# Kernel optimization log

Hardware: AMD Instinct MI355X
Metric: run time of the kernel (lower is better)

Reference implementation:

```python
import jax, jax.numpy as jnp
import numpy as np

EPS = 1e-5
HEADS = 4
DQK = 128
DV = 128
SCALE = DQK ** -0.5


def _bn(x, g, b, m, v):
    # inference-mode BatchNorm over channel dim (axis=1)
    inv = g / jnp.sqrt(v + EPS)
    return x * inv[None, :, None, None] + (b - m * inv)[None, :, None, None]


def setup_inputs() -> dict:
    key = jax.random.key(0)
    ks = jax.random.split(key, 16)
    f = lambda i, shape, s=1.0: jax.random.normal(ks[i], shape, dtype=jnp.float32) * s
    N, Cin, H, W = 16, 2048, 32, 32
    mid = HEADS * DV  # 512
    return {
        "x": f(0, (N, Cin, H, W)),
        "conv1_w": f(1, (mid, Cin), 0.02),
        "gamma1": 1.0 + f(2, (mid,), 0.02),
        "beta1": f(3, (mid,), 0.02),
        "mean1": f(4, (mid,), 0.02),
        "var1": 1.0 + 0.1 * jax.random.uniform(ks[5], (mid,), dtype=jnp.float32),
        "qk_w": f(6, (2 * HEADS * DQK, mid), 0.02),
        "v_w": f(7, (HEADS * DV, mid), 0.02),
        "pos_h": f(8, (H, DQK), SCALE),
        "pos_w": f(9, (W, DQK), SCALE),
        "conv3_w": f(10, (Cin, mid), 0.02),
        "gamma3": 1.0 + f(11, (Cin,), 0.02),
        "beta3": f(12, (Cin,), 0.02),
        "mean3": f(13, (Cin,), 0.02),
        "var3": 1.0 + 0.1 * jax.random.uniform(ks[14], (Cin,), dtype=jnp.float32),
    }


def reference(x, conv1_w, gamma1, beta1, mean1, var1, qk_w, v_w, pos_h, pos_w,
              conv3_w, gamma3, beta3, mean3, var3):
    n, c, h, w = x.shape
    # conv1 (1x1) + BN + ReLU
    out = jnp.einsum('nchw,oc->nohw', x, conv1_w)
    out = jax.nn.relu(_bn(out, gamma1, beta1, mean1, var1))
    # MHSA
    qk = jnp.einsum('nchw,oc->nohw', out, qk_w)  # [n, 2*heads*dqk, h, w]
    vv = jnp.einsum('nchw,oc->nohw', out, v_w)   # [n, heads*dv, h, w]
    q, k = jnp.split(qk, 2, axis=1)

    def to_heads(t):
        d = t.shape[1] // HEADS
        return t.reshape(n, HEADS, d, h * w).transpose(0, 1, 3, 2)  # [n, H, hw, d]

    q, k, vv = to_heads(q), to_heads(k), to_heads(vv)
    q = q * SCALE
    # absolute positional embedding: emb[(h w), d]
    emb = (pos_h[:, None, :] + pos_w[None, :, :]).reshape(h * w, DQK)
    logits = jnp.einsum('nhxd,nhyd->nhxy', q, k) + jnp.einsum('nhxd,yd->nhxy', q, emb)
    weights = jax.nn.softmax(logits, axis=-1)
    attn = jnp.einsum('nhxy,nhyd->nhxd', weights, vv)  # [n, H, hw, dv]
    attn = attn.transpose(0, 1, 3, 2).reshape(n, HEADS * DV, h, w)
    # stride=1 -> avg_pool is identity
    attn = jax.nn.relu(attn)
    # conv3 (1x1) + BN
    out = jnp.einsum('nchw,oc->nohw', attn, conv3_w)
    out = _bn(out, gamma3, beta3, mean3, var3)
    # residual (downsample=None, in==out channels, stride=1) + ReLU
    return jax.nn.relu(out + x)
```

## Files before the change

kernel.cpp:

```cpp
#include <hip/hip_runtime.h>
#include <stdint.h>

typedef __bf16 bf16_t;
typedef __bf16 bf16x8 __attribute__((ext_vector_type(8)));
typedef float f32x4 __attribute__((ext_vector_type(4)));

#define EPSV 1e-5f
#define QSCALE 0.08838834764831845f
#define NB 16
#define HWD 1024
#define CIN 2048
#define MID 512
#define QKLD 1024

__device__ __forceinline__ void gl_lds16(const bf16_t* g, void* l) {
    __builtin_amdgcn_global_load_lds(
        (const __attribute__((address_space(1))) uint32_t*)g,
        (__attribute__((address_space(3))) uint32_t*)l, 16, 0, 0);
}

__device__ __forceinline__ f32x4 mfma16(bf16x8 a, bf16x8 b, f32x4 c) {
    return __builtin_amdgcn_mfma_f32_16x16x32_bf16(a, b, c, 0, 0, 0);
}

#define PW1 (512*2048)
#define PQK (PW1 + 1024*512)
#define PV  (PQK + 512*512)
#define PW3 (PV  + 2048*512)
#define PE  (PW3 + 1024*128)

__global__ void prep_kernel(const float* __restrict__ conv1_w,
                            const float* __restrict__ qk_w,
                            const float* __restrict__ v_w,
                            const float* __restrict__ pos_h,
                            const float* __restrict__ pos_w,
                            const float* __restrict__ conv3_w,
                            bf16_t* __restrict__ w1b, bf16_t* __restrict__ wqkb,
                            bf16_t* __restrict__ wvb, bf16_t* __restrict__ w3b,
                            float* __restrict__ emb) {
    int stride = gridDim.x * blockDim.x;
    for (int i = blockIdx.x * blockDim.x + threadIdx.x; i < PE; i += stride) {
        if (i < PW1) {
            w1b[i] = (bf16_t)conv1_w[i];
        } else if (i < PQK) {
            int j = i - PW1;
            int row = j >> 9;
            float v = (row < 512) ? qk_w[j] * QSCALE : qk_w[j];
            wqkb[j] = (bf16_t)v;
        } else if (i < PV) {
            int j = i - PQK;
            wvb[j] = (bf16_t)v_w[j];
        } else if (i < PW3) {
            int j = i - PV;
            w3b[j] = (bf16_t)conv3_w[j];
        } else {
            int j = i - PW3;
            int y = j >> 7, d = j & 127;
            emb[j] = pos_h[(y >> 5) * 128 + d] + pos_w[(y & 31) * 128 + d];
        }
    }
}

__global__ void transpose_x_kernel(const float* __restrict__ x, bf16_t* __restrict__ xt) {
    __shared__ uint32_t tileT[64][20];
    const int n = blockIdx.z;
    const int c0 = blockIdx.x * 32;
    const int hw0 = blockIdx.y * 64;
    const int t = threadIdx.x;

    const int cp = t >> 4;
    const int hw4 = (t & 15) * 4;
    const float* p0 = x + ((size_t)n * CIN + c0 + 2 * cp) * HWD + hw0 + hw4;
    const float4 a = *(const float4*)p0;
    const float4 b = *(const float4*)(p0 + HWD);
    float av[4] = {a.x, a.y, a.z, a.w};
    float bv[4] = {b.x, b.y, b.z, b.w};
#pragma unroll
    for (int i = 0; i < 4; ++i) {
        uint16_t lo = __builtin_bit_cast(uint16_t, (bf16_t)av[i]);
        uint16_t hi = __builtin_bit_cast(uint16_t, (bf16_t)bv[i]);
        tileT[hw4 + i][cp] = (uint32_t)lo | ((uint32_t)hi << 16);
    }
    __syncthreads();
    const int hw = t >> 2;
    const int seg = (t & 3) * 4;
    uint4 v = *(const uint4*)&tileT[hw][seg];
    *(uint4*)(xt + ((size_t)n * HWD + hw0 + hw) * CIN + c0 + 2 * seg) = v;
}

template <int EPI>
__global__ __launch_bounds__(256, 4)
void gemm_bt(const bf16_t* __restrict__ A, long long aStride,
             const bf16_t* __restrict__ B, long long bStride,
             int K, int ldc,
             const float* __restrict__ e0, const float* __restrict__ e1,
             const float* __restrict__ e2, const float* __restrict__ e3,
             const float* __restrict__ e4, long long e4Stride,
             void* __restrict__ C, long long cStride) {
    __shared__ f32x4 smemv[2048];
    char* smem = (char*)smemv;
    bf16_t* As = (bf16_t*)smem;
    bf16_t* Bs = (bf16_t*)(smem + 16384);
    const int lane = threadIdx.x & 63;
    const int wave = threadIdx.x >> 6;
    const int tN = blockIdx.x * 128, tM = blockIdx.y * 128;
    const int b = blockIdx.z;
    A += (size_t)b * aStride;
    B += (size_t)b * bStride;

    const int wm = (wave >> 1) * 64, wn = (wave & 1) * 64;
    const int lrow = lane & 15, quad = lane >> 4;
    const int srow = lane >> 3;
    const int sgr = lane & 7;
    const int lg = sgr ^ srow;

    f32x4 acc[4][4];
    const f32x4 z4 = {0.f, 0.f, 0.f, 0.f};
#pragma unroll
    for (int i = 0; i < 4; ++i)
#pragma unroll
        for (int j = 0; j < 4; ++j) acc[i][j] = z4;

    for (int k0 = 0; k0 < K; k0 += 64) {
        __syncthreads();
#pragma unroll
        for (int j = 0; j < 4; ++j) {
            const int blk = wave * 4 + j;
            const int row = blk * 8 + srow;
            gl_lds16(A + (size_t)(tM + row) * K + k0 + lg * 8,
                     (char*)As + blk * 1024 + lane * 16);
            gl_lds16(B + (size_t)(tN + row) * K + k0 + lg * 8,
                     (char*)Bs + blk * 1024 + lane * 16);
        }
        __syncthreads();
#pragma unroll
        for (int kh = 0; kh < 2; ++kh) {
            bf16x8 af[4], bfr[4];
#pragma unroll
            for (int t = 0; t < 4; ++t) {
                const int ar = wm + t * 16 + lrow;
                af[t] = *(const bf16x8*)(As + ar * 64 + (((kh * 4 + quad) ^ (ar & 7)) * 8));
                const int br = wn + t * 16 + lrow;
                bfr[t] = *(const bf16x8*)(Bs + br * 64 + (((kh * 4 + quad) ^ (br & 7)) * 8));
            }
#pragma unroll
            for (int i = 0; i < 4; ++i)
#pragma unroll
                for (int j = 0; j < 4; ++j)
                    acc[i][j] = mfma16(af[i], bfr[j], acc[i][j]);
        }
    }

    __syncthreads();
    float* Es = (float*)(smem + wave * 4352);
    const int pr = lane >> 3;
    const int pc = (lane & 7) * 8;
    const int gcol = tN + wn + pc;

#pragma unroll
    for (int i = 0; i < 4; ++i) {
#pragma unroll
        for (int j = 0; j < 4; ++j)
#pragma unroll
            for (int r = 0; r < 4; ++r)
                Es[(quad * 4 + r) * 68 + j * 16 + lrow] = acc[i][j][r];
#pragma unroll
        for (int p = 0; p < 2; ++p) {
            const int lr = p * 8 + pr;
            const int grow = tM + wm + i * 16 + lr;
            float vf[8];
            *(f32x4*)&vf[0] = *(const f32x4*)&Es[lr * 68 + pc];
            *(f32x4*)&vf[4] = *(const f32x4*)&Es[lr * 68 + pc + 4];

            if constexpr (EPI == 1) {
                float gg[8], bt[8], mm[8], vv[8];
                *(f32x4*)&gg[0] = *(const f32x4*)(e0 + gcol);
                *(f32x4*)&gg[4] = *(const f32x4*)(e0 + gcol + 4);
                *(f32x4*)&bt[0] = *(const f32x4*)(e1 + gcol);
                *(f32x4*)&bt[4] = *(const f32x4*)(e1 + gcol + 4);
                *(f32x4*)&mm[0] = *(const f32x4*)(e2 + gcol);
                *(f32x4*)&mm[4] = *(const f32x4*)(e2 + gcol + 4);
                *(f32x4*)&vv[0] = *(const f32x4*)(e3 + gcol);
                *(f32x4*)&vv[4] = *(const f32x4*)(e3 + gcol + 4);
                bf16x8 ob;
#pragma unroll
                for (int c = 0; c < 8; ++c) {
                    float inv = gg[c] * rsqrtf(vv[c] + EPSV);
                    float val = fmaxf(vf[c] * inv + (bt[c] - mm[c] * inv), 0.f);
                    ob[c] = (bf16_t)val;
                }
                bf16_t* Cb = (bf16_t*)C + (size_t)b * cStride;
                *(bf16x8*)(Cb + (size_t)grow * ldc + gcol) = ob;
            } else if constexpr (EPI == 2) {
                bf16x8 ob;
                if (gcol >= 512) {
                    float ev[8];
                    const float* ep = e4 + (size_t)grow * 128 + (gcol & 127);
                    *(f32x4*)&ev[0] = *(const f32x4*)ep;
                    *(f32x4*)&ev[4] = *(const f32x4*)(ep + 4);
#pragma unroll
                    for (int c = 0; c < 8; ++c) ob[c] = (bf16_t)(vf[c] + ev[c]);
                } else {
#pragma unroll
                    for (int c = 0; c < 8; ++c) ob[c] = (bf16_t)vf[c];
                }
                bf16_t* Cb = (bf16_t*)C + (size_t)b * cStride;
                *(bf16x8*)(Cb + (size_t)grow * ldc + gcol) = ob;
            } else if constexpr (EPI == 4) {
                bf16x8 ob;
#pragma unroll
                for (int c = 0; c < 8; ++c) ob[c] = (bf16_t)vf[c];
                bf16_t* Cb = (bf16_t*)C + (size_t)b * cStride;
                *(bf16x8*)(Cb + (size_t)grow * ldc + gcol) = ob;
            } else {
                float g = e0[grow], bet = e1[grow], mn = e2[grow], vr = e3[grow];
                float inv = g * rsqrtf(vr + EPSV);
                float bbv = bet - mn * inv;
                const float* xr = e4 + (size_t)b * e4Stride + (size_t)grow * ldc + gcol;
                f32x4 x0 = *(const f32x4*)xr;
                f32x4 x1 = *(const f32x4*)(xr + 4);
                f32x4 o0, o1;
#pragma unroll
                for (int c = 0; c < 4; ++c) {
                    o0[c] = fmaxf(vf[c] * inv + bbv + x0[c], 0.f);
                    o1[c] = fmaxf(vf[c + 4] * inv + bbv + x1[c], 0.f);
                }
                float* Cf = (float*)C + (size_t)b * cStride + (size_t)grow * ldc + gcol;
                *(f32x4*)Cf = o0;
                *(f32x4*)(Cf + 4) = o1;
            }
        }
    }
}

__global__ __launch_bounds__(256, 2)
void attn_kernel(const bf16_t* __restrict__ qkt, const bf16_t* __restrict__ vt,
                 bf16_t* __restrict__ attn) {
    __shared__ bf16_t Ks[64 * 128];
    __shared__ bf16_t Vs[128 * 64];
    __shared__ bf16_t Ps[4 * 32 * 64];
    const int lane = threadIdx.x & 63;
    const int wave = threadIdx.x >> 6;
    const int qb = blockIdx.x, h = blockIdx.y, n = blockIdx.z;
    const int lrow = lane & 15, quad = lane >> 4;
    const int q0 = qb * 128 + wave * 32;

    bf16x8 qf[2][4];
#pragma unroll
    for (int rt = 0; rt < 2; ++rt)
#pragma unroll
        for (int kf = 0; kf < 4; ++kf)
            qf[rt][kf] = *(const bf16x8*)(qkt + (size_t)(n * HWD + q0 + rt * 16 + lrow) * QKLD
                                          + h * 128 + kf * 32 + quad * 8);

    f32x4 o[2][8];
    const f32x4 z4 = {0.f, 0.f, 0.f, 0.f};
#pragma unroll
    for (int rt = 0; rt < 2; ++rt)
#pragma unroll
        for (int d = 0; d < 8; ++d) o[rt][d] = z4;
    float l[2][4];
#pragma unroll
    for (int rt = 0; rt < 2; ++rt)
#pragma unroll
        for (int r = 0; r < 4; ++r) l[rt][r] = 0.f;

    const bf16_t* kbase = qkt + (size_t)n * HWD * QKLD + 512 + h * 128;
    const bf16_t* vbase = vt + (size_t)((n * 4 + h) * 128) * HWD;

    for (int kc = 0; kc < 16; ++kc) {
        __syncthreads();
#pragma unroll
        for (int j = 0; j < 4; ++j) {
            const int g = wave * 4 + j;
            const int krow = g * 4 + quad;
            const int kgl = lrow ^ (krow & 15);
            gl_lds16(kbase + (size_t)(kc * 64 + krow) * QKLD + kgl * 8,
                     (char*)Ks + g * 1024 + lane * 16);
            const int vrow = g * 8 + (lane >> 3);
            const int vgl = (lane & 7) ^ (vrow & 7);
            gl_lds16(vbase + (size_t)vrow * HWD + kc * 64 + vgl * 8,
                     (char*)Vs + g * 1024 + lane * 16);
        }
        __syncthreads();

        f32x4 s[2][4];
#pragma unroll
        for (int rt = 0; rt < 2; ++rt)
#pragma unroll
            for (int ct = 0; ct < 4; ++ct) s[rt][ct] = z4;
#pragma unroll
        for (int kf = 0; kf < 4; ++kf) {
#pragma unroll
            for (int ct = 0; ct < 4; ++ct) {
                bf16x8 kfrag = *(const bf16x8*)(Ks + (ct * 16 + lrow) * 128
                                                + ((kf * 4 + quad) ^ lrow) * 8);
                s[0][ct] = mfma16(qf[0][kf], kfrag, s[0][ct]);
                s[1][ct] = mfma16(qf[1][kf], kfrag, s[1][ct]);
            }
        }

#pragma unroll
        for (int rt = 0; rt < 2; ++rt) {
#pragma unroll
            for (int r = 0; r < 4; ++r) {
                const int prow = rt * 16 + quad * 4 + r;
                float rs = 0.f;
#pragma unroll
                for (int ct = 0; ct < 4; ++ct) {
                    float p = __expf(s[rt][ct][r]);
                    rs += p;
                    const int pg = (ct * 2 + (lrow >> 3)) ^ (prow & 7);
                    Ps[wave * 2048 + prow * 64 + pg * 8 + (lrow & 7)] = (bf16_t)p;
                }
                l[rt][r] += rs;
            }
        }
        asm volatile("s_waitcnt lgkmcnt(0)" ::: "memory");

#pragma unroll
        for (int kf = 0; kf < 2; ++kf) {
            bf16x8 pa0 = *(const bf16x8*)(Ps + wave * 2048 + lrow * 64
                                          + ((kf * 4 + quad) ^ (lrow & 7)) * 8);
            bf16x8 pa1 = *(const bf16x8*)(Ps + wave * 2048 + (16 + lrow) * 64
                                          + ((kf * 4 + quad) ^ (lrow & 7)) * 8);
#pragma unroll
            for (int d = 0; d < 8; ++d) {
                bf16x8 vf = *(const bf16x8*)(Vs + (d * 16 + lrow) * 64
                                             + ((kf * 4 + quad) ^ (lrow & 7)) * 8);
                o[0][d] = mfma16(pa0, vf, o[0][d]);
                o[1][d] = mfma16(pa1, vf, o[1][d]);
            }
        }
    }

#pragma unroll
    for (int rt = 0; rt < 2; ++rt)
#pragma unroll
        for (int r = 0; r < 4; ++r) {
#pragma unroll
            for (int off = 1; off < 16; off <<= 1)
                l[rt][r] += __shfl_xor(l[rt][r], off, 64);
        }

#pragma unroll
    for (int rt = 0; rt < 2; ++rt) {
#pragma unroll
        for (int r = 0; r < 4; ++r) {
            float linv = 1.f / l[rt][r];
            const size_t row = (size_t)n * HWD + q0 + rt * 16 + quad * 4 + r;
#pragma unroll
            for (int d = 0; d < 8; ++d) {
                float v = o[rt][d][r] * linv;
                v = fmaxf(v, 0.f);
                attn[row * MID + h * 128 + d * 16 + lrow] = (bf16_t)v;
            }
        }
    }
}

extern "C" void kernel_launch(void* const* d_in, const int* in_sizes, int n_in,
                              void* d_out, int out_size, void* d_ws, size_t ws_size,
                              hipStream_t stream) {
    const float* x       = (const float*)d_in[0];
    const float* conv1_w = (const float*)d_in[1];
    const float* gamma1  = (const float*)d_in[2];
    const float* beta1   = (const float*)d_in[3];
    const float* mean1   = (const float*)d_in[4];
    const float* var1    = (const float*)d_in[5];
    const float* qk_w    = (const float*)d_in[6];
    const float* v_w     = (const float*)d_in[7];
    const float* pos_h   = (const float*)d_in[8];
    const float* pos_w   = (const float*)d_in[9];
    const float* conv3_w = (const float*)d_in[10];
    const float* gamma3  = (const float*)d_in[11];
    const float* beta3   = (const float*)d_in[12];
    const float* mean3   = (const float*)d_in[13];
    const float* var3    = (const float*)d_in[14];
    float* out = (float*)d_out;

    char* ws = (char*)d_ws;
    size_t off = 0;
    auto carve = [&](size_t bytes) {
        void* p = ws + off;
        off += (bytes + 255) & ~(size_t)255;
        return p;
    };
    bf16_t* Xt    = (bf16_t*)carve((size_t)NB * HWD * CIN * 2);
    bf16_t* C1t   = (bf16_t*)carve((size_t)NB * HWD * MID * 2);
    bf16_t* QKt   = (bf16_t*)carve((size_t)NB * HWD * QKLD * 2);
    bf16_t* Vt    = (bf16_t*)carve((size_t)NB * 512 * HWD * 2);
    bf16_t* AttnT = (bf16_t*)carve((size_t)NB * HWD * MID * 2);
    bf16_t* W1b   = (bf16_t*)carve((size_t)512 * 2048 * 2);
    bf16_t* Wqkb  = (bf16_t*)carve((size_t)1024 * 512 * 2);
    bf16_t* Wvb   = (bf16_t*)carve((size_t)512 * 512 * 2);
    bf16_t* W3b   = (bf16_t*)carve((size_t)2048 * 512 * 2);
    float*  Emb   = (float*)carve((size_t)1024 * 128 * 4);

    prep_kernel<<<2048, 256, 0, stream>>>(conv1_w, qk_w, v_w, pos_h, pos_w, conv3_w,
                                          W1b, Wqkb, Wvb, W3b, Emb);

    transpose_x_kernel<<<dim3(64, 16, NB), 256, 0, stream>>>(x, Xt);

    gemm_bt<1><<<dim3(4, 8, NB), 256, 0, stream>>>(
        Xt, (long long)HWD * CIN, W1b, 0, CIN, MID,
        gamma1, beta1, mean1, var1, nullptr, 0, C1t, (long long)HWD * MID);

    gemm_bt<2><<<dim3(8, 8, NB), 256, 0, stream>>>(
        C1t, (long long)HWD * MID, Wqkb, 0, MID, QKLD,
        nullptr, nullptr, nullptr, nullptr, Emb, 0, QKt, (long long)HWD * QKLD);

    gemm_bt<4><<<dim3(8, 4, NB), 256, 0, stream>>>(
        Wvb, 0, C1t, (long long)HWD * MID, MID, HWD,
        nullptr, nullptr, nullptr, nullptr, nullptr, 0, Vt, (long long)512 * HWD);

    attn_kernel<<<dim3(8, 4, NB), 256, 0, stream>>>(QKt, Vt, AttnT);

    gemm_bt<3><<<dim3(8, 16, NB), 256, 0, stream>>>(
        W3b, 0, AttnT, (long long)HWD * MID, MID, HWD,
        gamma3, beta3, mean3, var3, x, (long long)CIN * HWD, out, (long long)CIN * HWD);
}
```

Measured before the change: 468.4 us.

## Double-buffer GEMM LDS tiles and prefetch residual input before main loop

The GEMM main loop now uses two LDS buffers, issuing global-to-LDS loads for the next K tile before computing on the current one, with explicit vmcnt waits and barriers. This is meant to hide global memory latency behind MFMA work. In the final residual epilogue, the x tile is loaded into registers before the K loop so its latency overlaps compute. The LDS size doubles and occupancy bounds drop from 4 to 2 blocks per CU, and the 16-register prefetch array raises register pressure.

```diff
diff --git a/kernel.cpp b/kernel.cpp
--- a/kernel.cpp
+++ b/kernel.cpp
@@ -89,7 +89,7 @@
 }
 
 template <int EPI>
-__global__ __launch_bounds__(256, 4)
+__global__ __launch_bounds__(256, 2)
 void gemm_bt(const bf16_t* __restrict__ A, long long aStride,
              const bf16_t* __restrict__ B, long long bStride,
              int K, int ldc,
@@ -97,10 +97,8 @@
              const float* __restrict__ e2, const float* __restrict__ e3,
              const float* __restrict__ e4, long long e4Stride,
              void* __restrict__ C, long long cStride) {
-    __shared__ f32x4 smemv[2048];
+    __shared__ f32x4 smemv[4096];
     char* smem = (char*)smemv;
-    bf16_t* As = (bf16_t*)smem;
-    bf16_t* Bs = (bf16_t*)(smem + 16384);
     const int lane = threadIdx.x & 63;
     const int wave = threadIdx.x >> 6;
     const int tN = blockIdx.x * 128, tM = blockIdx.y * 128;
@@ -114,6 +112,10 @@
     const int sgr = lane & 7;
     const int lg = sgr ^ srow;
 
+    const int pr = lane >> 3;
+    const int pc = (lane & 7) * 8;
+    const int gcol = tN + wn + pc;
+
     f32x4 acc[4][4];
     const f32x4 z4 = {0.f, 0.f, 0.f, 0.f};
 #pragma unroll
@@ -121,27 +123,55 @@
 #pragma unroll
         for (int j = 0; j < 4; ++j) acc[i][j] = z4;
 
-    for (int k0 = 0; k0 < K; k0 += 64) {
-        __syncthreads();
+    auto stage = [&](int buf, int k0) {
+        char* As_ = smem + buf * 32768;
+        char* Bs_ = As_ + 16384;
 #pragma unroll
         for (int j = 0; j < 4; ++j) {
             const int blk = wave * 4 + j;
             const int row = blk * 8 + srow;
             gl_lds16(A + (size_t)(tM + row) * K + k0 + lg * 8,
-                     (char*)As + blk * 1024 + lane * 16);
+                     As_ + blk * 1024 + lane * 16);
             gl_lds16(B + (size_t)(tN + row) * K + k0 + lg * 8,
-                     (char*)Bs + blk * 1024 + lane * 16);
-        }
-        __syncthreads();
+                     Bs_ + blk * 1024 + lane * 16);
+        }
+    };
+
+    f32x4 xpre[16];
+    if constexpr (EPI == 3) {
+        const float* xr = e4 + (size_t)b * e4Stride;
+#pragma unroll
+        for (int i = 0; i < 4; ++i)
+#pragma unroll
+            for (int p = 0; p < 2; ++p) {
+                const int grow = tM + wm + i * 16 + p * 8 + pr;
+                xpre[(i * 2 + p) * 2 + 0] = *(const f32x4*)(xr + (size_t)grow * ldc + gcol);
+                xpre[(i * 2 + p) * 2 + 1] = *(const f32x4*)(xr + (size_t)grow * ldc + gcol + 4);
+            }
+    }
+
+    const int nt = K >> 6;
+    stage(0, 0);
+
+    for (int t = 0; t < nt; ++t) {
+        const int cur = t & 1;
+        if (t + 1 < nt) {
+            stage(cur ^ 1, (t + 1) << 6);
+            asm volatile("s_waitcnt vmcnt(8)\n\ts_barrier" ::: "memory");
+        } else {
+            asm volatile("s_waitcnt vmcnt(0)\n\ts_barrier" ::: "memory");
+        }
+        const bf16_t* Asc = (const bf16_t*)(smem + cur * 32768);
+        const bf16_t* Bsc = (const bf16_t*)(smem + cur * 32768 + 16384);
 #pragma unroll
         for (int kh = 0; kh < 2; ++kh) {
             bf16x8 af[4], bfr[4];
 #pragma unroll
-            for (int t = 0; t < 4; ++t) {
-                const int ar = wm + t * 16 + lrow;
-                af[t] = *(const bf16x8*)(As + ar * 64 + (((kh * 4 + quad) ^ (ar & 7)) * 8));
-                const int br = wn + t * 16 + lrow;
-                bfr[t] = *(const bf16x8*)(Bs + br * 64 + (((kh * 4 + quad) ^ (br & 7)) * 8));
+            for (int t4 = 0; t4 < 4; ++t4) {
+                const int ar = wm + t4 * 16 + lrow;
+                af[t4] = *(const bf16x8*)(Asc + ar * 64 + (((kh * 4 + quad) ^ (ar & 7)) * 8));
+                const int br = wn + t4 * 16 + lrow;
+                bfr[t4] = *(const bf16x8*)(Bsc + br * 64 + (((kh * 4 + quad) ^ (br & 7)) * 8));
             }
 #pragma unroll
             for (int i = 0; i < 4; ++i)
@@ -149,13 +179,11 @@
                 for (int j = 0; j < 4; ++j)
                     acc[i][j] = mfma16(af[i], bfr[j], acc[i][j]);
         }
+        asm volatile("s_barrier" ::: "memory");
     }
 
     __syncthreads();
     float* Es = (float*)(smem + wave * 4352);
-    const int pr = lane >> 3;
-    const int pc = (lane & 7) * 8;
-    const int gcol = tN + wn + pc;
 
 #pragma unroll
     for (int i = 0; i < 4; ++i) {
@@ -216,9 +244,8 @@
                 float g = e0[grow], bet = e1[grow], mn = e2[grow], vr = e3[grow];
                 float inv = g * rsqrtf(vr + EPSV);
                 float bbv = bet - mn * inv;
-                const float* xr = e4 + (size_t)b * e4Stride + (size_t)grow * ldc + gcol;
-                f32x4 x0 = *(const f32x4*)xr;
-                f32x4 x1 = *(const f32x4*)(xr + 4);
+                f32x4 x0 = xpre[(i * 2 + p) * 2 + 0];
+                f32x4 x1 = xpre[(i * 2 + p) * 2 + 1];
                 f32x4 o0, o1;
 #pragma unroll
                 for (int c = 0; c < 4; ++c) {
```

New measurement: 471.7 us. About the same (+0.7%).
